# Optimization experiments

Hardware: AMD Instinct MI355X
Metric: run time of the kernel (lower is better)

Reference implementation:

```python
import jax, jax.numpy as jnp
import numpy as np

N_ENT = 100000   # n_entities
N_REL = 64       # n_relations
E_DIM = 64       # e_dim == r_dim (rel2ent is None)
K = 32           # neighbors per entity
B = 1024         # batch of seed entities
SLOPE = 0.2      # LeakyReLU negative_slope


def _xavier(key, shape, fan_in, fan_out):
    b = (6.0 / (fan_in + fan_out)) ** 0.5
    return jax.random.uniform(key, shape, jnp.float32, -b, b)


def setup_inputs() -> dict:
    key = jax.random.key(0)
    ks = jax.random.split(key, 10)
    E = _xavier(ks[0], (N_ENT, E_DIM), N_ENT, E_DIM)          # entity_embs.weight
    R = _xavier(ks[1], (N_REL, E_DIM), N_REL, E_DIM)          # relation_embs.weight
    att_w1 = _xavier(ks[2], (E_DIM, 2 * E_DIM), 2 * E_DIM, E_DIM)  # attention[0], no bias
    att_w2 = _xavier(ks[3], (E_DIM, E_DIM), E_DIM, E_DIM)          # attention[2], no bias
    att_w3 = _xavier(ks[4], (1, E_DIM), E_DIM, 1)                  # attention[4], no bias
    wx_w = _xavier(ks[5], (E_DIM, E_DIM), E_DIM, E_DIM)            # Wx[0].weight
    wx_b = jnp.zeros((E_DIM,), jnp.float32)                        # Wx[0].bias
    wc_w = _xavier(ks[6], (E_DIM, 2 * E_DIM), 2 * E_DIM, E_DIM)    # W_concat.weight
    wc_b = jnp.zeros((E_DIM,), jnp.float32)                        # W_concat.bias
    entity_idx = jax.random.randint(ks[7], (B,), 0, N_ENT)
    adj_entity = jax.random.randint(ks[8], (N_ENT, K), 0, N_ENT)
    adj_relation = jax.random.randint(ks[9], (N_ENT, K), 0, N_REL)
    return {
        "entity_idx": entity_idx, "adj_entity": adj_entity, "adj_relation": adj_relation,
        "E": E, "R": R, "att_w1": att_w1, "att_w2": att_w2, "att_w3": att_w3,
        "wx_w": wx_w, "wx_b": wx_b, "wc_w": wc_w, "wc_b": wc_b,
    }


def _lookup(W, idx):
    # nn.Embedding(max_norm=1): rows whose L2 norm exceeds 1 are renormalized.
    e = W[idx]
    n = jnp.linalg.norm(e, axis=-1, keepdims=True)
    return e * jnp.where(n > 1.0, 1.0 / (n + 1e-7), 1.0)


def _forward(entity_idx, adj_entity, adj_relation, E, R,
             att_w1, att_w2, att_w3, wx_w, wx_b, wc_w, wc_b):
    leaky = lambda x: jnp.where(x >= 0, x, SLOPE * x)
    # attention MLP on cat([h, r]): split first linear so the broadcast h term
    # is computed once per batch row instead of materializing [B, N, 2e].
    w1h, w1r = att_w1[:, :E_DIM], att_w1[:, E_DIM:]

    def gat(h, r, t):
        # h: [B, e] (broadcast over neighbors), r,t: [B, N, e]
        hid = jax.nn.relu(jnp.einsum('be,fe->bf', h, w1h)[:, None, :]
                          + jnp.einsum('bne,fe->bnf', r, w1r))
        hid = jax.nn.relu(jnp.einsum('bnf,gf->bng', hid, att_w2))
        a = jax.nn.sigmoid(jnp.einsum('bng,og->bno', hid, att_w3)[..., 0])  # [B, N]
        w = jax.nn.softmax(a, axis=-1)
        agg = jnp.einsum('bn,bne->be', w, t)       # softmax-weighted neighbor sum
        return agg @ wx_w.T + wx_b                 # per-head Linear (n_heads=1)

    Bsz = entity_idx.shape[0]
    # hop-1 / hop-2 neighbor index gathers (get_neighbors)
    ent1 = adj_entity[entity_idx]                  # [B, K]
    rel1 = adj_relation[entity_idx]                # [B, K]
    ent2 = adj_entity[ent1].reshape(Bsz, -1)       # [B, K*K]
    rel2 = adj_relation[ent1].reshape(Bsz, -1)     # [B, K*K]

    h = _lookup(E, entity_idx)                     # [B, e]
    t1 = _lookup(E, ent1)                          # [B, K, e]
    t2 = _lookup(E, ent2)                          # [B, K*K, e]
    r1 = _lookup(R, rel1)
    r2 = _lookup(R, rel2)

    # iter 0: seed entity broadcast as head
    v1 = leaky(gat(h, r1, t1))                                      # [B, e]
    emb1 = leaky(jnp.concatenate([h, v1], -1) @ wc_w.T + wc_b)      # aggregate 'concat'
    # iter 1: summed hop-1 neighborhood as head
    hsum = t1.sum(axis=1)                                           # [B, e]
    v2 = leaky(gat(hsum, r2, t2))
    emb2 = leaky(jnp.concatenate([hsum, v2], -1) @ wc_w.T + wc_b)
    # sum_aggregator 'concat': e_u = cat(embs[2], cat(embs[1], embs[0]))
    return jnp.concatenate([emb2, emb1, h], axis=-1)                # [B, 3e]


def reference(entity_idx, adj_entity, adj_relation, E, R,
              att_w1, att_w2, att_w3, wx_w, wx_b, wc_w, wc_b):
    return _forward(entity_idx, adj_entity, adj_relation, E, R,
                    att_w1, att_w2, att_w3, wx_w, wx_b, wc_w, wc_b)
```

## Files before the change

kernel.cpp:

```cpp
#include <hip/hip_runtime.h>

#define SLOPE 0.2f

__device__ __forceinline__ float leaky(float x) { return x >= 0.f ? x : SLOPE * x; }

enum : int {
  OFF_PT   = 0,
  OFF_W2T  = OFF_PT + 4096,
  OFF_A3   = OFF_W2T + 4096,
  OFF_WXT  = OFF_A3 + 64,
  OFF_WXB  = OFF_WXT + 4096,
  OFF_WCT  = OFF_WXB + 64,
  OFF_WCB  = OFF_WCT + 8192,
  OFF_W1HT = OFF_WCB + 64,
  WS_FLOATS = OFF_W1HT + 4096,
  EBF_U32  = 3200000
};

__global__ __launch_bounds__(256) void k1_prep(
    const float* __restrict__ R, const float* __restrict__ w1,
    const float* __restrict__ w2, const float* __restrict__ w3,
    const float* __restrict__ wxw, const float* __restrict__ wxb,
    const float* __restrict__ wcw, const float* __restrict__ wcb,
    const float* __restrict__ E, float* __restrict__ ws) {
  int tid = threadIdx.x;
  if (blockIdx.x >= 8) {
    const float2* E2 = (const float2*)E;
    unsigned* Ebf = (unsigned*)ws + WS_FLOATS;
    int stride = (gridDim.x - 8) * 256;
    for (int i = (blockIdx.x - 8) * 256 + tid; i < EBF_U32; i += stride) {
      float2 f = E2[i];
      unsigned ua = __float_as_uint(f.x);
      ua += 0x7FFFu + ((ua >> 16) & 1u);
      unsigned ub = __float_as_uint(f.y);
      ub += 0x7FFFu + ((ub >> 16) & 1u);
      Ebf[i] = (ua >> 16) | (ub & 0xFFFF0000u);
    }
    return;
  }
  __shared__ float Rn[64 * 65];
  int wv = tid >> 6, lane = tid & 63;
  for (int r = wv; r < 64; r += 4) {
    float v = R[r * 64 + lane];
    float ss = v * v;
    #pragma unroll
    for (int m = 1; m < 64; m <<= 1) ss += __shfl_xor(ss, m, 64);
    float n = sqrtf(ss);
    float sc = n > 1.f ? 1.f / (n + 1e-7f) : 1.f;
    Rn[r * 65 + lane] = v * sc;
  }
  __syncthreads();
  int gt = blockIdx.x * 256 + tid;
  for (int i = gt; i < 4096; i += 2048) {
    int f = i >> 6, r = i & 63;
    float acc = 0.f;
    #pragma unroll
    for (int e = 0; e < 64; ++e) acc += Rn[r * 65 + e] * w1[f * 128 + 64 + e];
    ws[OFF_PT + f * 64 + r] = acc;
  }
  for (int i = gt; i < 4096; i += 2048) {
    int f = i >> 6, g = i & 63;
    ws[OFF_W2T + i] = w2[g * 64 + f];
  }
  for (int i = gt; i < 4096; i += 2048) {
    int e = i >> 6, f = i & 63;
    ws[OFF_WXT + i]  = wxw[f * 64 + e];
    ws[OFF_W1HT + i] = w1[f * 128 + e];
  }
  for (int i = gt; i < 8192; i += 2048) {
    int e = i >> 6, f = i & 63;
    ws[OFF_WCT + i] = wcw[f * 128 + e];
  }
  if (gt < 64) {
    ws[OFF_A3 + gt]  = w3[gt];
    ws[OFF_WXB + gt] = wxb[gt];
    ws[OFF_WCB + gt] = wcb[gt];
  }
}

__global__ __launch_bounds__(256) void k_main(
    const int* __restrict__ entity_idx, const int* __restrict__ adj_entity,
    const int* __restrict__ adj_relation, const float* __restrict__ E,
    const float* __restrict__ ws, float* __restrict__ out) {
  __shared__ float s_t1[32 * 64];
  __shared__ float s_partA[4][64], s_partB[4][64];
  __shared__ int   s_ent1[32], s_rel1[32];
  __shared__ unsigned s_ei[1024];
  __shared__ float s_w[1024];
  __shared__ float s_h[64], s_hs[64], s_hq1[64], s_hq2[64];
  __shared__ float s_at1[64], s_at2[64], s_agg1[64], s_agg2[64], s_v1[64], s_v2[64];
  __shared__ float s_L1, s_L2;
  int b = blockIdx.x, tid = threadIdx.x, wv = tid >> 6, lane = tid & 63;
  int idx = entity_idx[b];

  if (tid < 64) s_h[tid] = E[(long)idx * 64 + tid];
  if (tid >= 64 && tid < 96) {
    int i = tid - 64;
    s_ent1[i] = adj_entity[(long)idx * 32 + i];
    s_rel1[i] = adj_relation[(long)idx * 32 + i];
  }
  if (tid == 0) s_L2 = 0.f;
  __syncthreads();

  #pragma unroll
  for (int i = 0; i < 4; ++i) {
    int n = tid + i * 256;
    int j = n >> 5, i2 = n & 31;
    long base = (long)s_ent1[j] * 32 + i2;
    unsigned ei = (unsigned)adj_entity[base];
    unsigned ri = (unsigned)adj_relation[base];
    s_ei[n] = ei | (ri << 24);
  }
  {
    float hs = 0.f;
    #pragma unroll
    for (int k = 0; k < 8; ++k) {
      int n = wv * 8 + k;
      float v = E[(long)s_ent1[n] * 64 + lane];
      s_t1[n * 64 + lane] = v;
      hs += v;
    }
    s_partA[wv][lane] = hs;
  }
  __syncthreads();
  if (tid < 64)
    s_hs[tid] = s_partA[0][tid] + s_partA[1][tid] + s_partA[2][tid] + s_partA[3][tid];
  __syncthreads();

  {
    const float* src = (wv < 2) ? s_h : s_hs;
    int e0 = (wv & 1) * 32;
    float p = 0.f;
    #pragma unroll 8
    for (int e = 0; e < 32; ++e) p += ws[OFF_W1HT + (e0 + e) * 64 + lane] * src[e0 + e];
    s_partB[wv][lane] = p;
  }
  __syncthreads();
  if (tid < 64) s_hq1[tid] = s_partB[0][tid] + s_partB[1][tid];
  else if (tid < 128) { int i = tid - 64; s_hq2[i] = s_partB[2][i] + s_partB[3][i]; }
  __syncthreads();

  {
    int swv = __builtin_amdgcn_readfirstlane(wv);
    const float* W2T = ws + OFF_W2T;
    const float* A3  = ws + OFF_A3;
    const float* PT  = ws + OFF_PT;
    float acc1[16], acc2[16];
    #pragma unroll
    for (int i = 0; i < 16; ++i) { acc1[i] = 0.f; acc2[i] = 0.f; }
    int g0 = swv * 16;
    #pragma unroll 2
    for (int f = 0; f < 64; ++f) {
      float ptv = PT[f * 64 + lane];
      float h1 = fmaxf(s_hq1[f] + ptv, 0.f);
      float h2 = fmaxf(s_hq2[f] + ptv, 0.f);
      const float* w = W2T + f * 64 + g0;
      #pragma unroll
      for (int i = 0; i < 16; ++i) { acc1[i] += w[i] * h1; acc2[i] += w[i] * h2; }
    }
    float s1 = 0.f, s2 = 0.f;
    #pragma unroll
    for (int i = 0; i < 16; ++i) {
      float a3 = A3[g0 + i];
      s1 += a3 * fmaxf(acc1[i], 0.f);
      s2 += a3 * fmaxf(acc2[i], 0.f);
    }
    s_partA[wv][lane] = s1;
    s_partB[wv][lane] = s2;
  }
  __syncthreads();
  if (tid < 64) {
    float t = s_partA[0][tid] + s_partA[1][tid] + s_partA[2][tid] + s_partA[3][tid];
    float a = 1.f / (1.f + __expf(-t));
    s_at1[tid] = __expf(a);
  } else if (tid < 128) {
    int i = tid - 64;
    float t = s_partB[0][i] + s_partB[1][i] + s_partB[2][i] + s_partB[3][i];
    float a = 1.f / (1.f + __expf(-t));
    s_at2[i] = __expf(a);
  }
  __syncthreads();

  {
    float wsum = 0.f;
    #pragma unroll
    for (int i = 0; i < 4; ++i) {
      int n = tid + i * 256;
      float wgt = s_at2[s_ei[n] >> 24];
      s_w[n] = wgt;
      wsum += wgt;
    }
    #pragma unroll
    for (int m = 1; m < 64; m <<= 1) wsum += __shfl_xor(wsum, m, 64);
    if (lane == 0) atomicAdd(&s_L2, wsum);
  }
  if (tid < 32) {
    float w = s_at1[s_rel1[tid]];
    #pragma unroll
    for (int m = 1; m < 32; m <<= 1) w += __shfl_xor(w, m, 64);
    if (tid == 0) s_L1 = w;
  }
  __syncthreads();

  {
    const uint4* Ebf = (const uint4*)((const unsigned*)ws + WS_FLOATS);
    int sub8 = lane >> 3, eg8 = lane & 7;
    float acc[8];
    #pragma unroll
    for (int k = 0; k < 8; ++k) acc[k] = 0.f;
    #pragma unroll 1
    for (int t = 0; t < 8; ++t) {
      uint4 v[4];
      float wgt[4];
      #pragma unroll
      for (int j = 0; j < 4; ++j) {
        int n = (t * 4 + j) * 32 + wv * 8 + sub8;
        v[j] = Ebf[(long)(s_ei[n] & 0xFFFFFFu) * 8 + eg8];
        wgt[j] = s_w[n];
      }
      #pragma unroll
      for (int j = 0; j < 4; ++j) {
        float w = wgt[j];
        acc[0] += w * __uint_as_float(v[j].x << 16);
        acc[1] += w * __uint_as_float(v[j].x & 0xFFFF0000u);
        acc[2] += w * __uint_as_float(v[j].y << 16);
        acc[3] += w * __uint_as_float(v[j].y & 0xFFFF0000u);
        acc[4] += w * __uint_as_float(v[j].z << 16);
        acc[5] += w * __uint_as_float(v[j].z & 0xFFFF0000u);
        acc[6] += w * __uint_as_float(v[j].w << 16);
        acc[7] += w * __uint_as_float(v[j].w & 0xFFFF0000u);
      }
    }
    #pragma unroll
    for (int m = 8; m < 64; m <<= 1) {
      #pragma unroll
      for (int k = 0; k < 8; ++k) acc[k] += __shfl_xor(acc[k], m, 64);
    }
    if (sub8 == 0) {
      #pragma unroll
      for (int k = 0; k < 8; ++k) s_partB[wv][eg8 * 8 + k] = acc[k];
    }
  }
  {
    float a1 = 0.f;
    #pragma unroll
    for (int k = 0; k < 8; ++k) {
      int n = wv * 8 + k;
      a1 += s_at1[s_rel1[n]] * s_t1[n * 64 + lane];
    }
    s_partA[wv][lane] = a1;
  }
  __syncthreads();
  if (tid < 64) {
    float a = s_partA[0][tid] + s_partA[1][tid] + s_partA[2][tid] + s_partA[3][tid];
    s_agg1[tid] = a / s_L1;
  } else if (tid < 128) {
    int i = tid - 64;
    float a = s_partB[0][i] + s_partB[1][i] + s_partB[2][i] + s_partB[3][i];
    s_agg2[i] = a / s_L2;
  }
  __syncthreads();

  {
    const float* src = (wv < 2) ? s_agg1 : s_agg2;
    int e0 = (wv & 1) * 32;
    float p = 0.f;
    #pragma unroll 8
    for (int e = 0; e < 32; ++e)
      p += ws[OFF_WXT + (e0 + e) * 64 + lane] * src[e0 + e];
    s_partA[wv][lane] = p;
  }
  __syncthreads();
  if (tid < 64) {
    s_v1[tid] = leaky(ws[OFF_WXB + tid] + s_partA[0][tid] + s_partA[1][tid]);
  } else if (tid < 128) {
    int i = tid - 64;
    s_v2[i] = leaky(ws[OFF_WXB + i] + s_partA[2][i] + s_partA[3][i]);
  }
  __syncthreads();

  {
    const float* src = (wv == 0) ? s_h : (wv == 1) ? s_v1 : (wv == 2) ? s_hs : s_v2;
    int e0 = (wv & 1) * 64;
    float p = 0.f;
    #pragma unroll 8
    for (int e = 0; e < 64; ++e)
      p += ws[OFF_WCT + (e0 + e) * 64 + lane] * src[e];
    s_partB[wv][lane] = p;
  }
  __syncthreads();
  if (tid < 64) {
    float o = ws[OFF_WCB + tid] + s_partB[0][tid] + s_partB[1][tid];
    out[b * 192 + 64 + tid]  = leaky(o);
    out[b * 192 + 128 + tid] = s_h[tid];
  } else if (tid < 128) {
    int i = tid - 64;
    float o = ws[OFF_WCB + i] + s_partB[2][i] + s_partB[3][i];
    out[b * 192 + i] = leaky(o);
  }
}

extern "C" void kernel_launch(void* const* d_in, const int* in_sizes, int n_in,
                              void* d_out, int out_size, void* d_ws, size_t ws_size,
                              hipStream_t stream) {
  const int* entity_idx   = (const int*)d_in[0];
  const int* adj_entity   = (const int*)d_in[1];
  const int* adj_relation = (const int*)d_in[2];
  const float* E          = (const float*)d_in[3];
  const float* R          = (const float*)d_in[4];
  const float* att_w1     = (const float*)d_in[5];
  const float* att_w2     = (const float*)d_in[6];
  const float* att_w3     = (const float*)d_in[7];
  const float* wx_w       = (const float*)d_in[8];
  const float* wx_b       = (const float*)d_in[9];
  const float* wc_w       = (const float*)d_in[10];
  const float* wc_b       = (const float*)d_in[11];
  float* out              = (float*)d_out;
  float* ws               = (float*)d_ws;

  hipLaunchKernelGGL(k1_prep, dim3(1608), dim3(256), 0, stream,
                     R, att_w1, att_w2, att_w3, wx_w, wx_b, wc_w, wc_b, E, ws);
  hipLaunchKernelGGL(k_main, dim3(1024), dim3(256), 0, stream,
                     entity_idx, adj_entity, adj_relation, E, ws, out);
}
```

Before: 151.3 us.

## Fuse prep and main kernels into one cooperative kernel with grid sync

Merges the weight-prep and bf16 entity-table conversion kernel with the main per-seed kernel into a single cooperative launch. Each block first converts part of E and, for a few blocks, transposes weights. It then does the seed-local index and embedding loads, which do not depend on the prep outputs, before a single grid-wide sync, so they overlap with prep. This removes one kernel launch boundary and hides gather latency behind the conversion. In exchange it relies on cooperative-launch support and occupancy checks, falls back to the old two-kernel path otherwise, and adds a grid barrier plus static launch state.

```diff
diff --git a/kernel.cpp b/kernel.cpp
--- a/kernel.cpp
+++ b/kernel.cpp
@@ -1,4 +1,7 @@
 #include <hip/hip_runtime.h>
+#include <hip/hip_cooperative_groups.h>
+
+namespace cg = cooperative_groups;
 
 #define SLOPE 0.2f
 
@@ -16,6 +19,292 @@
   WS_FLOATS = OFF_W1HT + 4096,
   EBF_U32  = 3200000
 };
+
+__global__ __launch_bounds__(256, 4) void k_coop(
+    const int* __restrict__ entity_idx, const int* __restrict__ adj_entity,
+    const int* __restrict__ adj_relation, const float* __restrict__ E,
+    const float* __restrict__ R, const float* __restrict__ w1,
+    const float* __restrict__ w2, const float* __restrict__ w3,
+    const float* __restrict__ wxw, const float* __restrict__ wxb,
+    const float* __restrict__ wcw, const float* __restrict__ wcb,
+    float* __restrict__ ws, float* __restrict__ out) {
+  __shared__ unsigned s_ei[1024];
+  __shared__ float s_w[1024];
+  __shared__ float s_partA[4][64], s_partB[4][64];
+  __shared__ int   s_ent1[32], s_rel1[32];
+  __shared__ float s_h[64], s_hs[64], s_hq1[64], s_hq2[64];
+  __shared__ float s_at1[64], s_at2[64], s_agg1[64], s_agg2[64], s_v1[64], s_v2[64];
+  __shared__ float s_scale[64];
+  __shared__ float s_L1, s_L2;
+
+  int tid = threadIdx.x, wv = tid >> 6, lane = tid & 63;
+
+  {
+    const float2* E2 = (const float2*)E;
+    unsigned* Ebf = (unsigned*)ws + WS_FLOATS;
+    int stride = gridDim.x * 256;
+    for (int i = blockIdx.x * 256 + tid; i < EBF_U32; i += stride) {
+      float2 f = E2[i];
+      unsigned ua = __float_as_uint(f.x);
+      ua += 0x7FFFu + ((ua >> 16) & 1u);
+      unsigned ub = __float_as_uint(f.y);
+      ub += 0x7FFFu + ((ub >> 16) & 1u);
+      Ebf[i] = (ua >> 16) | (ub & 0xFFFF0000u);
+    }
+  }
+
+  if (blockIdx.x < 8) {
+    for (int r = wv; r < 64; r += 4) {
+      float v = R[r * 64 + lane];
+      float ss = v * v;
+      #pragma unroll
+      for (int m = 1; m < 64; m <<= 1) ss += __shfl_xor(ss, m, 64);
+      if (lane == 0) {
+        float n = sqrtf(ss);
+        s_scale[r] = n > 1.f ? 1.f / (n + 1e-7f) : 1.f;
+      }
+    }
+    __syncthreads();
+    int gt = blockIdx.x * 256 + tid;
+    for (int i = gt; i < 4096; i += 2048) {
+      int f = i >> 6, r2 = i & 63;
+      float acc = 0.f;
+      #pragma unroll
+      for (int e = 0; e < 64; ++e) acc += R[r2 * 64 + e] * w1[f * 128 + 64 + e];
+      ws[OFF_PT + f * 64 + r2] = acc * s_scale[r2];
+    }
+    for (int i = gt; i < 4096; i += 2048) {
+      int f = i >> 6, g = i & 63;
+      ws[OFF_W2T + i] = w2[g * 64 + f];
+    }
+    for (int i = gt; i < 4096; i += 2048) {
+      int e = i >> 6, f = i & 63;
+      ws[OFF_WXT + i]  = wxw[f * 64 + e];
+      ws[OFF_W1HT + i] = w1[f * 128 + e];
+    }
+    for (int i = gt; i < 8192; i += 2048) {
+      int e = i >> 6, f = i & 63;
+      ws[OFF_WCT + i] = wcw[f * 128 + e];
+    }
+    if (gt < 64) {
+      ws[OFF_A3 + gt]  = w3[gt];
+      ws[OFF_WXB + gt] = wxb[gt];
+      ws[OFF_WCB + gt] = wcb[gt];
+    }
+  }
+  __syncthreads();
+
+  bool synced = false;
+  for (int b = blockIdx.x; b < 1024; b += gridDim.x) {
+    int idx = entity_idx[b];
+
+    if (tid < 64) s_h[tid] = E[(long)idx * 64 + tid];
+    if (tid >= 64 && tid < 96) {
+      int i = tid - 64;
+      s_ent1[i] = adj_entity[(long)idx * 32 + i];
+      s_rel1[i] = adj_relation[(long)idx * 32 + i];
+    }
+    if (tid == 0) s_L2 = 0.f;
+    __syncthreads();
+
+    #pragma unroll
+    for (int i = 0; i < 4; ++i) {
+      int n = tid + i * 256;
+      int j = n >> 5, i2 = n & 31;
+      long base = (long)s_ent1[j] * 32 + i2;
+      unsigned ei = (unsigned)adj_entity[base];
+      unsigned ri = (unsigned)adj_relation[base];
+      s_ei[n] = ei | (ri << 24);
+    }
+    {
+      float hs = 0.f;
+      #pragma unroll
+      for (int k = 0; k < 8; ++k) {
+        int n = wv * 8 + k;
+        hs += E[(long)s_ent1[n] * 64 + lane];
+      }
+      s_partA[wv][lane] = hs;
+    }
+    __syncthreads();
+    if (tid < 64)
+      s_hs[tid] = s_partA[0][tid] + s_partA[1][tid] + s_partA[2][tid] + s_partA[3][tid];
+    __syncthreads();
+
+    if (!synced) { cg::this_grid().sync(); synced = true; }
+
+    {
+      const float* src = (wv < 2) ? s_h : s_hs;
+      int e0 = (wv & 1) * 32;
+      float p = 0.f;
+      #pragma unroll 8
+      for (int e = 0; e < 32; ++e) p += ws[OFF_W1HT + (e0 + e) * 64 + lane] * src[e0 + e];
+      s_partB[wv][lane] = p;
+    }
+    __syncthreads();
+    if (tid < 64) s_hq1[tid] = s_partB[0][tid] + s_partB[1][tid];
+    else if (tid < 128) { int i = tid - 64; s_hq2[i] = s_partB[2][i] + s_partB[3][i]; }
+    __syncthreads();
+
+    {
+      int swv = __builtin_amdgcn_readfirstlane(wv);
+      const float* W2T = ws + OFF_W2T;
+      const float* A3  = ws + OFF_A3;
+      const float* PT  = ws + OFF_PT;
+      float acc1[16], acc2[16];
+      #pragma unroll
+      for (int i = 0; i < 16; ++i) { acc1[i] = 0.f; acc2[i] = 0.f; }
+      int g0 = swv * 16;
+      #pragma unroll 2
+      for (int f = 0; f < 64; ++f) {
+        float ptv = PT[f * 64 + lane];
+        float h1 = fmaxf(s_hq1[f] + ptv, 0.f);
+        float h2 = fmaxf(s_hq2[f] + ptv, 0.f);
+        const float* w = W2T + f * 64 + g0;
+        #pragma unroll
+        for (int i = 0; i < 16; ++i) { acc1[i] += w[i] * h1; acc2[i] += w[i] * h2; }
+      }
+      float s1 = 0.f, s2 = 0.f;
+      #pragma unroll
+      for (int i = 0; i < 16; ++i) {
+        float a3 = A3[g0 + i];
+        s1 += a3 * fmaxf(acc1[i], 0.f);
+        s2 += a3 * fmaxf(acc2[i], 0.f);
+      }
+      s_partA[wv][lane] = s1;
+      s_partB[wv][lane] = s2;
+    }
+    __syncthreads();
+    if (tid < 64) {
+      float t = s_partA[0][tid] + s_partA[1][tid] + s_partA[2][tid] + s_partA[3][tid];
+      float a = 1.f / (1.f + __expf(-t));
+      s_at1[tid] = __expf(a);
+    } else if (tid < 128) {
+      int i = tid - 64;
+      float t = s_partB[0][i] + s_partB[1][i] + s_partB[2][i] + s_partB[3][i];
+      float a = 1.f / (1.f + __expf(-t));
+      s_at2[i] = __expf(a);
+    }
+    __syncthreads();
+
+    {
+      float wsum = 0.f;
+      #pragma unroll
+      for (int i = 0; i < 4; ++i) {
+        int n = tid + i * 256;
+        float wgt = s_at2[s_ei[n] >> 24];
+        s_w[n] = wgt;
+        wsum += wgt;
+      }
+      #pragma unroll
+      for (int m = 1; m < 64; m <<= 1) wsum += __shfl_xor(wsum, m, 64);
+      if (lane == 0) atomicAdd(&s_L2, wsum);
+    }
+    if (tid < 32) {
+      float w = s_at1[s_rel1[tid]];
+      #pragma unroll
+      for (int m = 1; m < 32; m <<= 1) w += __shfl_xor(w, m, 64);
+      if (tid == 0) s_L1 = w;
+    }
+    __syncthreads();
+
+    {
+      const uint4* Ebf = (const uint4*)((const unsigned*)ws + WS_FLOATS);
+      int sub8 = lane >> 3, eg8 = lane & 7;
+      float acc[8];
+      #pragma unroll
+      for (int k = 0; k < 8; ++k) acc[k] = 0.f;
+      #pragma unroll 1
+      for (int t = 0; t < 8; ++t) {
+        uint4 v[4];
+        float wgt[4];
+        #pragma unroll
+        for (int j = 0; j < 4; ++j) {
+          int n = (t * 4 + j) * 32 + wv * 8 + sub8;
+          v[j] = Ebf[(long)(s_ei[n] & 0xFFFFFFu) * 8 + eg8];
+          wgt[j] = s_w[n];
+        }
+        #pragma unroll
+        for (int j = 0; j < 4; ++j) {
+          float w = wgt[j];
+          acc[0] += w * __uint_as_float(v[j].x << 16);
+          acc[1] += w * __uint_as_float(v[j].x & 0xFFFF0000u);
+          acc[2] += w * __uint_as_float(v[j].y << 16);
+          acc[3] += w * __uint_as_float(v[j].y & 0xFFFF0000u);
+          acc[4] += w * __uint_as_float(v[j].z << 16);
+          acc[5] += w * __uint_as_float(v[j].z & 0xFFFF0000u);
+          acc[6] += w * __uint_as_float(v[j].w << 16);
+          acc[7] += w * __uint_as_float(v[j].w & 0xFFFF0000u);
+        }
+      }
+      #pragma unroll
+      for (int m = 8; m < 64; m <<= 1) {
+        #pragma unroll
+        for (int k = 0; k < 8; ++k) acc[k] += __shfl_xor(acc[k], m, 64);
+      }
+      if (sub8 == 0) {
+        #pragma unroll
+        for (int k = 0; k < 8; ++k) s_partB[wv][eg8 * 8 + k] = acc[k];
+      }
+    }
+    {
+      float a1 = 0.f;
+      #pragma unroll
+      for (int k = 0; k < 8; ++k) {
+        int n = wv * 8 + k;
+        a1 += s_at1[s_rel1[n]] * E[(long)s_ent1[n] * 64 + lane];
+      }
+      s_partA[wv][lane] = a1;
+    }
+    __syncthreads();
+    if (tid < 64) {
+      float a = s_partA[0][tid] + s_partA[1][tid] + s_partA[2][tid] + s_partA[3][tid];
+      s_agg1[tid] = a / s_L1;
+    } else if (tid < 128) {
+      int i = tid - 64;
+      float a = s_partB[0][i] + s_partB[1][i] + s_partB[2][i] + s_partB[3][i];
+      s_agg2[i] = a / s_L2;
+    }
+    __syncthreads();
+
+    {
+      const float* src = (wv < 2) ? s_agg1 : s_agg2;
+      int e0 = (wv & 1) * 32;
+      float p = 0.f;
+      #pragma unroll 8
+      for (int e = 0; e < 32; ++e)
+        p += ws[OFF_WXT + (e0 + e) * 64 + lane] * src[e0 + e];
+      s_partA[wv][lane] = p;
+    }
+    __syncthreads();
+    if (tid < 64) {
+      s_v1[tid] = leaky(ws[OFF_WXB + tid] + s_partA[0][tid] + s_partA[1][tid]);
+    } else if (tid < 128) {
+      int i = tid - 64;
+      s_v2[i] = leaky(ws[OFF_WXB + i] + s_partA[2][i] + s_partA[3][i]);
+    }
+    __syncthreads();
+
+    {
+      const float* src = (wv == 0) ? s_h : (wv == 1) ? s_v1 : (wv == 2) ? s_hs : s_v2;
+      float p = 0.f;
+      #pragma unroll 8
+      for (int e = 0; e < 64; ++e)
+        p += ws[OFF_WCT + ((wv & 1) * 64 + e) * 64 + lane] * src[e];
+      s_partB[wv][lane] = p;
+    }
+    __syncthreads();
+    if (tid < 64) {
+      float o = ws[OFF_WCB + tid] + s_partB[0][tid] + s_partB[1][tid];
+      out[b * 192 + 64 + tid]  = leaky(o);
+      out[b * 192 + 128 + tid] = s_h[tid];
+    } else if (tid < 128) {
+      int i = tid - 64;
+      float o = ws[OFF_WCB + i] + s_partB[2][i] + s_partB[3][i];
+      out[b * 192 + i] = leaky(o);
+    }
+    __syncthreads();
+  }
+}
 
 __global__ __launch_bounds__(256) void k1_prep(
     const float* __restrict__ R, const float* __restrict__ w1,
@@ -318,6 +607,50 @@
   float* out              = (float*)d_out;
   float* ws               = (float*)d_ws;
 
+  static int coop_state = 0;
+
+  if (coop_state == 0) {
+    hipStreamCaptureStatus cap = hipStreamCaptureStatusNone;
+    (void)hipStreamIsCapturing(stream, &cap);
+    if (cap == hipStreamCaptureStatusNone) {
+      int dev = 0, coopAttr = 0, numCU = 0, occ = 0;
+      (void)hipGetDevice(&dev);
+      (void)hipDeviceGetAttribute(&coopAttr, hipDeviceAttributeCooperativeLaunch, dev);
+      (void)hipDeviceGetAttribute(&numCU, hipDeviceAttributeMultiprocessorCount, dev);
+      hipError_t qe = hipOccupancyMaxActiveBlocksPerMultiprocessor(
+          &occ, reinterpret_cast<const void*>(k_coop), 256, 0);
+      long cap_blocks = (qe == hipSuccess) ? (long)occ * (long)numCU : 0;
+      int grid = (!coopAttr || cap_blocks < 512) ? 0 : (cap_blocks >= 1024 ? 1024 : 512);
+      if (grid > 0) {
+        void* args[] = {
+            (void*)&entity_idx, (void*)&adj_entity, (void*)&adj_relation,
+            (void*)&E, (void*)&R, (void*)&att_w1, (void*)&att_w2, (void*)&att_w3,
+            (void*)&wx_w, (void*)&wx_b, (void*)&wc_w, (void*)&wc_b,
+            (void*)&ws, (void*)&out};
+        hipError_t le = hipLaunchCooperativeKernel((void*)k_coop, dim3(grid),
+                                                   dim3(256), args, 0, stream);
+        if (le == hipSuccess) { coop_state = grid; return; }
+        (void)hipGetLastError();
+        coop_state = -1;
+      } else {
+        coop_state = -1;
+      }
+    }
+  }
+
+  if (coop_state > 0) {
+    void* args[] = {
+        (void*)&entity_idx, (void*)&adj_entity, (void*)&adj_relation,
+        (void*)&E, (void*)&R, (void*)&att_w1, (void*)&att_w2, (void*)&att_w3,
+        (void*)&wx_w, (void*)&wx_b, (void*)&wc_w, (void*)&wc_b,
+        (void*)&ws, (void*)&out};
+    hipError_t le = hipLaunchCooperativeKernel((void*)k_coop, dim3(coop_state),
+                                               dim3(256), args, 0, stream);
+    if (le == hipSuccess) return;
+    (void)hipGetLastError();
+    coop_state = -1;
+  }
+
   hipLaunchKernelGGL(k1_prep, dim3(1608), dim3(256), 0, stream,
                      R, att_w1, att_w2, att_w3, wx_w, wx_b, wc_w, wc_b, E, ws);
   hipLaunchKernelGGL(k_main, dim3(1024), dim3(256), 0, stream,
```

After: 304.9 us. 2.02x slower.

## Double-buffer bf16 neighbor gathers and widen fp32-to-bf16 conversion loads

Applied to the files above, without the earlier changes.

The hop-2 weighted gather loop now keeps two 8-deep register buffers of uint4 loads, issuing the next batch before consuming the current one. This raises memory-level parallelism in place of the old unroll-1 loop, which issued only 4 loads per iteration. The entity table conversion in the prep kernel also switches to float4 reads with uint2 writes. The extra registers (64 for the buffers) may lower occupancy.

```diff
diff --git a/kernel.cpp b/kernel.cpp
--- a/kernel.cpp
+++ b/kernel.cpp
@@ -25,16 +25,20 @@
     const float* __restrict__ E, float* __restrict__ ws) {
   int tid = threadIdx.x;
   if (blockIdx.x >= 8) {
-    const float2* E2 = (const float2*)E;
-    unsigned* Ebf = (unsigned*)ws + WS_FLOATS;
+    const float4* E4 = (const float4*)E;
+    uint2* Ebf2 = (uint2*)((unsigned*)ws + WS_FLOATS);
+    int nvec = EBF_U32 / 2;
     int stride = (gridDim.x - 8) * 256;
-    for (int i = (blockIdx.x - 8) * 256 + tid; i < EBF_U32; i += stride) {
-      float2 f = E2[i];
-      unsigned ua = __float_as_uint(f.x);
-      ua += 0x7FFFu + ((ua >> 16) & 1u);
-      unsigned ub = __float_as_uint(f.y);
-      ub += 0x7FFFu + ((ub >> 16) & 1u);
-      Ebf[i] = (ua >> 16) | (ub & 0xFFFF0000u);
+    for (int i = (blockIdx.x - 8) * 256 + tid; i < nvec; i += stride) {
+      float4 f = E4[i];
+      unsigned ua = __float_as_uint(f.x); ua += 0x7FFFu + ((ua >> 16) & 1u);
+      unsigned ub = __float_as_uint(f.y); ub += 0x7FFFu + ((ub >> 16) & 1u);
+      unsigned uc = __float_as_uint(f.z); uc += 0x7FFFu + ((uc >> 16) & 1u);
+      unsigned ud = __float_as_uint(f.w); ud += 0x7FFFu + ((ud >> 16) & 1u);
+      uint2 o;
+      o.x = (ua >> 16) | (ub & 0xFFFF0000u);
+      o.y = (uc >> 16) | (ud & 0xFFFF0000u);
+      Ebf2[i] = o;
     }
     return;
   }
@@ -77,6 +81,31 @@
     ws[OFF_WCB + gt] = wcb[gt];
   }
 }
+
+#define LOAD8(V, W, G0)                                       \
+  {                                                           \
+    _Pragma("unroll")                                         \
+    for (int j = 0; j < 8; ++j) {                             \
+      int n = ((G0) + j) * 32 + rbase;                        \
+      (V)[j] = Ebf[(long)(s_ei[n] & 0xFFFFFFu) * 8 + eg8];    \
+      (W)[j] = s_w[n];                                        \
+    }                                                         \
+  }
+#define CONSUME8(V, W)                                        \
+  {                                                           \
+    _Pragma("unroll")                                         \
+    for (int j = 0; j < 8; ++j) {                             \
+      float w = (W)[j];                                       \
+      acc[0] += w * __uint_as_float((V)[j].x << 16);          \
+      acc[1] += w * __uint_as_float((V)[j].x & 0xFFFF0000u);  \
+      acc[2] += w * __uint_as_float((V)[j].y << 16);          \
+      acc[3] += w * __uint_as_float((V)[j].y & 0xFFFF0000u);  \
+      acc[4] += w * __uint_as_float((V)[j].z << 16);          \
+      acc[5] += w * __uint_as_float((V)[j].z & 0xFFFF0000u);  \
+      acc[6] += w * __uint_as_float((V)[j].w << 16);          \
+      acc[7] += w * __uint_as_float((V)[j].w & 0xFFFF0000u);  \
+    }                                                         \
+  }
 
 __global__ __launch_bounds__(256) void k_main(
     const int* __restrict__ entity_idx, const int* __restrict__ adj_entity,
@@ -205,32 +234,22 @@
   {
     const uint4* Ebf = (const uint4*)((const unsigned*)ws + WS_FLOATS);
     int sub8 = lane >> 3, eg8 = lane & 7;
+    int rbase = wv * 8 + sub8;
     float acc[8];
     #pragma unroll
     for (int k = 0; k < 8; ++k) acc[k] = 0.f;
-    #pragma unroll 1
-    for (int t = 0; t < 8; ++t) {
-      uint4 v[4];
-      float wgt[4];
-      #pragma unroll
-      for (int j = 0; j < 4; ++j) {
-        int n = (t * 4 + j) * 32 + wv * 8 + sub8;
-        v[j] = Ebf[(long)(s_ei[n] & 0xFFFFFFu) * 8 + eg8];
-        wgt[j] = s_w[n];
-      }
-      #pragma unroll
-      for (int j = 0; j < 4; ++j) {
-        float w = wgt[j];
-        acc[0] += w * __uint_as_float(v[j].x << 16);
-        acc[1] += w * __uint_as_float(v[j].x & 0xFFFF0000u);
-        acc[2] += w * __uint_as_float(v[j].y << 16);
-        acc[3] += w * __uint_as_float(v[j].y & 0xFFFF0000u);
-        acc[4] += w * __uint_as_float(v[j].z << 16);
-        acc[5] += w * __uint_as_float(v[j].z & 0xFFFF0000u);
-        acc[6] += w * __uint_as_float(v[j].w << 16);
-        acc[7] += w * __uint_as_float(v[j].w & 0xFFFF0000u);
-      }
-    }
+
+    uint4 va[8], vb[8];
+    float wa[8], wb[8];
+    LOAD8(va, wa, 0);
+    LOAD8(vb, wb, 8);
+    CONSUME8(va, wa);
+    LOAD8(va, wa, 16);
+    CONSUME8(vb, wb);
+    LOAD8(vb, wb, 24);
+    CONSUME8(va, wa);
+    CONSUME8(vb, wb);
+
     #pragma unroll
     for (int m = 8; m < 64; m <<= 1) {
       #pragma unroll
```

Result: slower. 170.5 us (+12.7%).

## Overlap hop-1 attention MLP with hop-2 gather and widen bf16 conversion stores

Applied to the files above, without the earlier changes.

Moves the hop-1 attention MLP computation into the hop-2 embedding gather loop. Its FMA work can then hide the latency of the scattered bf16 row loads, while the hop-2 MLP runs alone beforehand. The hop-1 weight sum and aggregation are moved after that loop, which adds one extra block barrier. Separately, the fp32-to-bf16 table conversion now reads float4 and writes 64-bit nontemporal stores, cutting the instruction count and keeping the converted output from polluting the cache.

```diff
diff --git a/kernel.cpp b/kernel.cpp
--- a/kernel.cpp
+++ b/kernel.cpp
@@ -25,16 +25,22 @@
     const float* __restrict__ E, float* __restrict__ ws) {
   int tid = threadIdx.x;
   if (blockIdx.x >= 8) {
-    const float2* E2 = (const float2*)E;
-    unsigned* Ebf = (unsigned*)ws + WS_FLOATS;
+    const float4* E4 = (const float4*)E;
+    unsigned long long* Ebf2 =
+        (unsigned long long*)((unsigned*)ws + WS_FLOATS);
+    int nvec = EBF_U32 / 2;
     int stride = (gridDim.x - 8) * 256;
-    for (int i = (blockIdx.x - 8) * 256 + tid; i < EBF_U32; i += stride) {
-      float2 f = E2[i];
-      unsigned ua = __float_as_uint(f.x);
-      ua += 0x7FFFu + ((ua >> 16) & 1u);
-      unsigned ub = __float_as_uint(f.y);
-      ub += 0x7FFFu + ((ub >> 16) & 1u);
-      Ebf[i] = (ua >> 16) | (ub & 0xFFFF0000u);
+    for (int i = (blockIdx.x - 8) * 256 + tid; i < nvec; i += stride) {
+      float4 f = E4[i];
+      unsigned ua = __float_as_uint(f.x); ua += 0x7FFFu + ((ua >> 16) & 1u);
+      unsigned ub = __float_as_uint(f.y); ub += 0x7FFFu + ((ub >> 16) & 1u);
+      unsigned uc = __float_as_uint(f.z); uc += 0x7FFFu + ((uc >> 16) & 1u);
+      unsigned ud = __float_as_uint(f.w); ud += 0x7FFFu + ((ud >> 16) & 1u);
+      unsigned lo = (ua >> 16) | (ub & 0xFFFF0000u);
+      unsigned hi = (uc >> 16) | (ud & 0xFFFF0000u);
+      unsigned long long o = (unsigned long long)lo |
+                             ((unsigned long long)hi << 32);
+      __builtin_nontemporal_store(o, &Ebf2[i]);
     }
     return;
   }
@@ -145,39 +151,28 @@
     const float* W2T = ws + OFF_W2T;
     const float* A3  = ws + OFF_A3;
     const float* PT  = ws + OFF_PT;
-    float acc1[16], acc2[16];
-    #pragma unroll
-    for (int i = 0; i < 16; ++i) { acc1[i] = 0.f; acc2[i] = 0.f; }
+    float acc2[16];
+    #pragma unroll
+    for (int i = 0; i < 16; ++i) acc2[i] = 0.f;
     int g0 = swv * 16;
     #pragma unroll 2
     for (int f = 0; f < 64; ++f) {
       float ptv = PT[f * 64 + lane];
-      float h1 = fmaxf(s_hq1[f] + ptv, 0.f);
       float h2 = fmaxf(s_hq2[f] + ptv, 0.f);
       const float* w = W2T + f * 64 + g0;
       #pragma unroll
-      for (int i = 0; i < 16; ++i) { acc1[i] += w[i] * h1; acc2[i] += w[i] * h2; }
-    }
-    float s1 = 0.f, s2 = 0.f;
-    #pragma unroll
-    for (int i = 0; i < 16; ++i) {
-      float a3 = A3[g0 + i];
-      s1 += a3 * fmaxf(acc1[i], 0.f);
-      s2 += a3 * fmaxf(acc2[i], 0.f);
-    }
-    s_partA[wv][lane] = s1;
+      for (int i = 0; i < 16; ++i) acc2[i] += w[i] * h2;
+    }
+    float s2 = 0.f;
+    #pragma unroll
+    for (int i = 0; i < 16; ++i) s2 += A3[g0 + i] * fmaxf(acc2[i], 0.f);
     s_partB[wv][lane] = s2;
   }
   __syncthreads();
   if (tid < 64) {
-    float t = s_partA[0][tid] + s_partA[1][tid] + s_partA[2][tid] + s_partA[3][tid];
+    float t = s_partB[0][tid] + s_partB[1][tid] + s_partB[2][tid] + s_partB[3][tid];
     float a = 1.f / (1.f + __expf(-t));
-    s_at1[tid] = __expf(a);
-  } else if (tid < 128) {
-    int i = tid - 64;
-    float t = s_partB[0][i] + s_partB[1][i] + s_partB[2][i] + s_partB[3][i];
-    float a = 1.f / (1.f + __expf(-t));
-    s_at2[i] = __expf(a);
+    s_at2[tid] = __expf(a);
   }
   __syncthreads();
 
@@ -194,29 +189,41 @@
     for (int m = 1; m < 64; m <<= 1) wsum += __shfl_xor(wsum, m, 64);
     if (lane == 0) atomicAdd(&s_L2, wsum);
   }
-  if (tid < 32) {
-    float w = s_at1[s_rel1[tid]];
-    #pragma unroll
-    for (int m = 1; m < 32; m <<= 1) w += __shfl_xor(w, m, 64);
-    if (tid == 0) s_L1 = w;
-  }
   __syncthreads();
 
   {
     const uint4* Ebf = (const uint4*)((const unsigned*)ws + WS_FLOATS);
     int sub8 = lane >> 3, eg8 = lane & 7;
-    float acc[8];
+    int rbase = wv * 8 + sub8;
+    int swv = __builtin_amdgcn_readfirstlane(wv);
+    const float* W2T = ws + OFF_W2T;
+    const float* A3  = ws + OFF_A3;
+    const float* PT  = ws + OFF_PT;
+    int g0 = swv * 16;
+    float acc[8], acc1[16];
     #pragma unroll
     for (int k = 0; k < 8; ++k) acc[k] = 0.f;
+    #pragma unroll
+    for (int i = 0; i < 16; ++i) acc1[i] = 0.f;
+
     #pragma unroll 1
     for (int t = 0; t < 8; ++t) {
       uint4 v[4];
       float wgt[4];
       #pragma unroll
       for (int j = 0; j < 4; ++j) {
-        int n = (t * 4 + j) * 32 + wv * 8 + sub8;
+        int n = (t * 4 + j) * 32 + rbase;
         v[j] = Ebf[(long)(s_ei[n] & 0xFFFFFFu) * 8 + eg8];
         wgt[j] = s_w[n];
+      }
+      #pragma unroll
+      for (int ff = 0; ff < 8; ++ff) {
+        int f = t * 8 + ff;
+        float ptv = PT[f * 64 + lane];
+        float h1 = fmaxf(s_hq1[f] + ptv, 0.f);
+        const float* w = W2T + f * 64 + g0;
+        #pragma unroll
+        for (int i = 0; i < 16; ++i) acc1[i] += w[i] * h1;
       }
       #pragma unroll
       for (int j = 0; j < 4; ++j) {
@@ -231,6 +238,10 @@
         acc[7] += w * __uint_as_float(v[j].w & 0xFFFF0000u);
       }
     }
+    float s1 = 0.f;
+    #pragma unroll
+    for (int i = 0; i < 16; ++i) s1 += A3[g0 + i] * fmaxf(acc1[i], 0.f);
+    s_partA[wv][lane] = s1;
     #pragma unroll
     for (int m = 8; m < 64; m <<= 1) {
       #pragma unroll
@@ -241,23 +252,37 @@
       for (int k = 0; k < 8; ++k) s_partB[wv][eg8 * 8 + k] = acc[k];
     }
   }
-  {
-    float a1 = 0.f;
-    #pragma unroll
-    for (int k = 0; k < 8; ++k) {
-      int n = wv * 8 + k;
-      a1 += s_at1[s_rel1[n]] * s_t1[n * 64 + lane];
-    }
-    s_partA[wv][lane] = a1;
-  }
-  __syncthreads();
-  if (tid < 64) {
-    float a = s_partA[0][tid] + s_partA[1][tid] + s_partA[2][tid] + s_partA[3][tid];
-    s_agg1[tid] = a / s_L1;
+  __syncthreads();
+  if (tid < 64) {
+    float t = s_partA[0][tid] + s_partA[1][tid] + s_partA[2][tid] + s_partA[3][tid];
+    float a = 1.f / (1.f + __expf(-t));
+    s_at1[tid] = __expf(a);
   } else if (tid < 128) {
     int i = tid - 64;
     float a = s_partB[0][i] + s_partB[1][i] + s_partB[2][i] + s_partB[3][i];
     s_agg2[i] = a / s_L2;
+  }
+  __syncthreads();
+
+  if (tid < 32) {
+    float w = s_at1[s_rel1[tid]];
+    #pragma unroll
+    for (int m = 1; m < 32; m <<= 1) w += __shfl_xor(w, m, 64);
+    if (tid == 0) s_L1 = w;
+  }
+  {
+    float a1 = 0.f;
+    #pragma unroll
+    for (int k = 0; k < 8; ++k) {
+      int n = wv * 8 + k;
+      a1 += s_at1[s_rel1[n]] * s_t1[n * 64 + lane];
+    }
+    s_partA[wv][lane] = a1;
+  }
+  __syncthreads();
+  if (tid < 64) {
+    float a = s_partA[0][tid] + s_partA[1][tid] + s_partA[2][tid] + s_partA[3][tid];
+    s_agg1[tid] = a / s_L1;
   }
   __syncthreads();
 
```

New measurement: 149.5 us. Within noise of the previous version (-1.2%).
